# Performance work log

Hardware: AMD Instinct MI355X
Metric: run time of the kernel (lower is better)

## Reference

```python
import jax, jax.numpy as jnp
import numpy as np

N_EMBD = 1024
HEAD_SIZE = 64

def setup_inputs() -> dict:
    key = jax.random.key(0)
    kx, kk, kq, kv = jax.random.split(key, 4)
    x = jax.random.normal(kx, (8, 2048, N_EMBD), dtype=jnp.float32)
    scale = 1.0 / np.sqrt(N_EMBD)
    # nn.Linear weights are [out, in]; kaiming-uniform-ish init
    Wk = jax.random.uniform(kk, (HEAD_SIZE, N_EMBD), dtype=jnp.float32, minval=-scale, maxval=scale)
    Wq = jax.random.uniform(kq, (HEAD_SIZE, N_EMBD), dtype=jnp.float32, minval=-scale, maxval=scale)
    Wv = jax.random.uniform(kv, (HEAD_SIZE, N_EMBD), dtype=jnp.float32, minval=-scale, maxval=scale)
    return {"x": x, "Wk": Wk, "Wq": Wq, "Wv": Wv}

def reference(x, Wk, Wq, Wv):
    # x: [B, T, E]; W*: [H, E] (torch Linear layout)
    k = jnp.einsum('bte,he->bth', x, Wk)
    q = jnp.einsum('bte,he->bth', x, Wq)
    v = jnp.einsum('bte,he->bth', x, Wv)
    inv_sqrt_h = 1.0 / np.sqrt(HEAD_SIZE)
    wei = jnp.einsum('bth,bsh->bts', q, k) * inv_sqrt_h  # [B, T, T]
    wei = jax.nn.softmax(wei, axis=-1)
    out = jnp.einsum('bts,bsh->bth', wei, v)  # [B, T, H]
    return out
```

## Files before the change

kernel.cpp:

```cpp
#include <hip/hip_runtime.h>
#include <cstdint>

#define NB 8
#define TS 2048
#define NE 1024
#define HD 64
#define MTOT (NB*TS)

typedef float     f4  __attribute__((ext_vector_type(4)));
typedef short     s8v __attribute__((ext_vector_type(8)));
typedef short     s4v __attribute__((ext_vector_type(4)));
typedef int       i4v __attribute__((ext_vector_type(4)));
typedef _Float16  h8  __attribute__((ext_vector_type(8)));

__device__ __forceinline__ short f2bf(float f) {
  union { float f; uint32_t u; } x; x.f = f;
  return (short)((x.u + 0x7FFFu + ((x.u >> 16) & 1u)) >> 16);
}

__device__ __forceinline__ int pack2(float lo, float hi) {
  union { float f; uint32_t u; } a, b; a.f = lo; b.f = hi;
  return (int)__builtin_amdgcn_perm(b.u + 0x8000u, a.u + 0x8000u, 0x07060302u);
}

__device__ __forceinline__ void gl2lds(const void* gptr, void* lptr) {
  auto g = (const __attribute__((address_space(1))) uint32_t*)gptr;
  auto l = (__attribute__((address_space(3))) uint32_t*)lptr;
  __builtin_amdgcn_global_load_lds(g, l, 16, 0, 0);
}

template <int N>
__device__ __forceinline__ void wait_barrier() {
  asm volatile("s_waitcnt vmcnt(%0) lgkmcnt(0)" :: "n"(N) : "memory");
  __builtin_amdgcn_s_barrier();
}

__global__ __launch_bounds__(256) void wconv_kernel(
    const float* __restrict__ Wk, const float* __restrict__ Wq, const float* __restrict__ Wv,
    short* __restrict__ wb)
{
  const int idx = (blockIdx.x * 256 + threadIdx.x) * 4;
  const int p = idx >> 16;
  const int off = idx & 65535;
  const float* W = (p == 0) ? Wq : (p == 1) ? Wk : Wv;
  const float s = (p == 0) ? 0.18033688011112042f : 1.0f;
  const float4 v = *(const float4*)&W[off];
  s4v h; h[0] = f2bf(v.x*s); h[1] = f2bf(v.y*s); h[2] = f2bf(v.z*s); h[3] = f2bf(v.w*s);
  *(s4v*)&wb[idx] = h;
}

__global__ __launch_bounds__(256) void proj_kernel(
    const float* __restrict__ x, const short* __restrict__ wb,
    short* __restrict__ qo, short* __restrict__ ko, _Float16* __restrict__ vo)
{
  __shared__ float Xs[4][32][64];
  __shared__ short Ws[2][192][64];
  const int tid = threadIdx.x;
  const int wv = tid >> 6, lane = tid & 63, n = lane & 15, quad = lane >> 4;
  const int mg = wv & 1, cg = wv >> 1;
  const int r0 = blockIdx.x * 32;
  const int xrow = lane >> 4, xslot = lane & 15;
  const int wrow = lane >> 3, wslot = lane & 7;

  auto dmaX = [&](int c, int buf) {
#pragma unroll
    for (int u = 0; u < 2; ++u) {
      const int R0 = (wv * 2 + u) * 4;
      const int row = R0 + xrow;
      const int gs = (xslot + row) & 15;
      gl2lds(&x[(size_t)(r0 + row) * NE + c * 64 + gs * 4], &Xs[buf][R0][0]);
    }
  };
  auto dmaW = [&](int c, int buf) {
#pragma unroll
    for (int u = 0; u < 6; ++u) {
      const int C0 = (wv * 6 + u) * 8;
      const int col = C0 + wrow;
      const int gs = (wslot + col) & 7;
      gl2lds(&wb[(size_t)col * NE + c * 64 + gs * 8], &Ws[buf][C0][0]);
    }
  };

  const f4 fz = {0.f, 0.f, 0.f, 0.f};
  f4 acc[6] = {fz, fz, fz, fz, fz, fz};

  auto compute = [&](int bw, int bx) {
    s8v a[2];
    const int row = mg * 16 + n;
#pragma unroll
    for (int kc = 0; kc < 2; ++kc) {
      const int u0 = kc * 8 + quad * 2;
      const float* pr = &Xs[bx][row][0];
      const f4 f0 = *(const f4*)(pr + (((u0    ) - row) & 15) * 4);
      const f4 f1 = *(const f4*)(pr + (((u0 + 1) - row) & 15) * 4);
      i4v ai;
      ai[0] = pack2(f0[0], f0[1]); ai[1] = pack2(f0[2], f0[3]);
      ai[2] = pack2(f1[0], f1[1]); ai[3] = pack2(f1[2], f1[3]);
      a[kc] = __builtin_bit_cast(s8v, ai);
    }
#pragma unroll
    for (int nf = 0; nf < 6; ++nf) {
      const int col = cg * 96 + nf * 16 + n;
      const s8v b0 = *(const s8v*)&Ws[bw][col][(((0 + quad) - col) & 7) * 8];
      const s8v b1 = *(const s8v*)&Ws[bw][col][(((4 + quad) - col) & 7) * 8];
      acc[nf] = __builtin_amdgcn_mfma_f32_16x16x32_bf16(a[0], b0, acc[nf], 0, 0, 0);
      acc[nf] = __builtin_amdgcn_mfma_f32_16x16x32_bf16(a[1], b1, acc[nf], 0, 0, 0);
    }
  };

  dmaW(0, 0); dmaX(0, 0); dmaX(1, 1); dmaX(2, 2);
  wait_barrier<4>();

  for (int t = 0; t < 16; ++t) {
    if (t <= 14) dmaW(t + 1, (t + 1) & 1);
    if (t <= 12) dmaX(t + 3, (t + 3) & 3);
    compute(t & 1, t & 3);
    if (t <= 12)      wait_barrier<2>();
    else if (t <= 14) wait_barrier<0>();
  }

#pragma unroll
  for (int nf = 0; nf < 6; ++nf) {
    const int gc = cg * 96 + nf * 16;
    const int p = gc >> 6;
    const int rcol = (gc & 63) + n;
#pragma unroll
    for (int i = 0; i < 4; ++i) {
      const int R = r0 + mg * 16 + quad * 4 + i;
      const float av = acc[nf][i];
      if (p == 0)      qo[(size_t)R * HD + rcol] = f2bf(av);
      else if (p == 1) ko[(size_t)R * HD + rcol] = f2bf(av);
      else {
        const int t2 = R & (TS - 1), b = t2 & 31;
        const int pos = (t2 & ~31) | (((b >> 2) & 3) << 3) | (((b >> 4) & 1) << 2) | (b & 3);
        vo[(size_t)(R >> 11) * HD * TS + (size_t)rcol * TS + pos] = (_Float16)av;
      }
    }
  }
}

__global__ __launch_bounds__(512) void attn_kernel(
    const short* __restrict__ q, const short* __restrict__ k,
    const _Float16* __restrict__ vT, float* __restrict__ out)
{
  __shared__ __align__(16) char smem[98304];
  const int tid = threadIdx.x;
  const int wv = tid >> 6, lane = tid & 63, n = lane & 15, quad = lane >> 4;
  const int half = wv >> 2, qw = wv & 3;
  const int batch = blockIdx.x & 7;
  const int qg = blockIdx.x >> 3;
  const int m0 = batch * TS + qg * 64;
  const short*    kb = k  + (size_t)batch * TS * HD;
  const _Float16* vb = vT + (size_t)batch * HD * TS;
  const int drow = lane >> 3, dslot = lane & 7;
  const f4 fz = {0.f, 0.f, 0.f, 0.f};

  auto kbuf = [&](int buf) { return (short*)   (smem +         (half * 3 + buf) * 8192); };
  auto vbuf = [&](int buf) { return (_Float16*)(smem + 49152 + (half * 3 + buf) * 8192); };

  auto dmaKV = [&](int tt, int buf) {
    const int c = half * 16 + tt;
#pragma unroll
    for (int u = 0; u < 2; ++u) {
      const int K0 = (qw * 2 + u) * 8;
      const int key = K0 + drow;
      const int gs = (dslot + key) & 7;
      gl2lds(&kb[(size_t)(c * 64 + key) * HD + gs * 8], kbuf(buf) + K0 * 64);
    }
#pragma unroll
    for (int u = 0; u < 2; ++u) {
      const int D0 = (qw * 2 + u) * 8;
      const int d = D0 + drow;
      const int gs = (dslot + d) & 7;
      gl2lds(&vb[(size_t)d * TS + c * 64 + gs * 8], vbuf(buf) + D0 * 64);
    }
  };

  s8v qf[2];
#pragma unroll
  for (int kc = 0; kc < 2; ++kc)
    qf[kc] = *(const s8v*)&q[(size_t)(m0 + qw * 16 + n) * HD + kc * 32 + quad * 8];

  f4 o[4] = {fz, fz, fz, fz};
  f4 lD = fz;
  h8 ones;
#pragma unroll
  for (int j = 0; j < 8; ++j) ones[j] = (_Float16)1.0f;

  dmaKV(0, 0); dmaKV(1, 1);
  wait_barrier<4>();

  for (int t = 0; t < 16; ++t) {
    const int buf = t % 3;
    if (t <= 13) dmaKV(t + 2, (t + 2) % 3);

    const short*    ks = kbuf(buf);
    const _Float16* vs = vbuf(buf);

    s8v kf[4][2];
#pragma unroll
    for (int f = 0; f < 4; ++f)
#pragma unroll
      for (int kc = 0; kc < 2; ++kc) {
        const int key = f * 16 + n;
        kf[f][kc] = *(const s8v*)&ks[key * 64 + (((kc * 4 + quad) - key) & 7) * 8];
      }

    f4 st[4];
#pragma unroll
    for (int f = 0; f < 4; ++f) {
      st[f] = __builtin_amdgcn_mfma_f32_16x16x32_bf16(kf[f][0], qf[0], fz, 0, 0, 0);
      st[f] = __builtin_amdgcn_mfma_f32_16x16x32_bf16(kf[f][1], qf[1], st[f], 0, 0, 0);
    }

    h8 pa[2];
#pragma unroll
    for (int pr = 0; pr < 2; ++pr)
#pragma unroll
      for (int hf = 0; hf < 2; ++hf)
#pragma unroll
        for (int i = 0; i < 4; ++i)
          pa[pr][hf * 4 + i] = (_Float16)__builtin_amdgcn_exp2f(st[pr * 2 + hf][i]);

#pragma unroll
    for (int pr = 0; pr < 2; ++pr) {
      lD = __builtin_amdgcn_mfma_f32_16x16x32_f16(pa[pr], ones, lD, 0, 0, 0);
#pragma unroll
      for (int g = 0; g < 4; ++g) {
        const int d = g * 16 + n;
        const h8 vf = *(const h8*)&vs[d * 64 + (((pr * 4 + quad) - d) & 7) * 8];
        o[g] = __builtin_amdgcn_mfma_f32_16x16x32_f16(pa[pr], vf, o[g], 0, 0, 0);
      }
    }

    if (t <= 13)      wait_barrier<4>();
    else if (t == 14) wait_barrier<0>();
  }

  __syncthreads();

  float* o_c = (float*)smem;
  float* l_c = (float*)(smem + 36864);
  if (n == 0)
#pragma unroll
    for (int i = 0; i < 4; ++i) l_c[wv * 16 + quad * 4 + i] = lD[i];
#pragma unroll
  for (int g = 0; g < 4; ++g)
#pragma unroll
    for (int i = 0; i < 4; ++i)
      o_c[(wv * 16 + quad * 4 + i) * 68 + g * 16 + n] = o[g][i];
  __syncthreads();

#pragma unroll
  for (int rep = 0; rep < 2; ++rep) {
    const int idx = tid + rep * 512;
    const int qr = idx >> 4, d4 = (idx & 15) * 4;
    const int qw2 = qr >> 4, wr = qr & 15;
    const float L = l_c[qw2 * 16 + wr] + l_c[(qw2 + 4) * 16 + wr];
    const f4 s0 = *(const f4*)&o_c[(qw2 * 16 + wr) * 68 + d4];
    const f4 s1 = *(const f4*)&o_c[((qw2 + 4) * 16 + wr) * 68 + d4];
    f4 r = (s0 + s1);
    const float inv = 1.0f / L;
    r[0] *= inv; r[1] *= inv; r[2] *= inv; r[3] *= inv;
    *(f4*)&out[(size_t)(m0 + qr) * HD + d4] = r;
  }
}

extern "C" void kernel_launch(void* const* d_in, const int* in_sizes, int n_in,
                              void* d_out, int out_size, void* d_ws, size_t ws_size,
                              hipStream_t stream) {
  const float* x  = (const float*)d_in[0];
  const float* Wk = (const float*)d_in[1];
  const float* Wq = (const float*)d_in[2];
  const float* Wv = (const float*)d_in[3];
  float* out = (float*)d_out;

  short* qb = (short*)d_ws;
  short* kb = qb + (size_t)MTOT * HD;
  _Float16* vb = (_Float16*)(kb + (size_t)MTOT * HD);
  short* wb = (short*)(vb + (size_t)NB * HD * TS);

  wconv_kernel<<<192, 256, 0, stream>>>(Wk, Wq, Wv, wb);
  proj_kernel<<<MTOT / 32, 256, 0, stream>>>(x, wb, qb, kb, vb);
  attn_kernel<<<MTOT / 64, 512, 0, stream>>>(qb, kb, vb, out);
}
```

Baseline: 129.5 us.

## Split keys four ways across wave pairs, each wave handling 32 query rows

Reorganizes the attention block so the 8 waves form 4 key-range quarters of 2 waves each. Each wave now owns 32 query rows and processes 32-key tiles instead of 16 rows by 64 keys. Each K/V fragment loaded from LDS is reused across two query row tiles, which halves per-wave LDS reads per MFMA and shrinks per-buffer staging. The cost is that the final reduction combines four partial outputs per row instead of two, and more registers are held for accumulators.

```diff
diff --git a/kernel.cpp b/kernel.cpp
--- a/kernel.cpp
+++ b/kernel.cpp
@@ -146,93 +146,99 @@
   __shared__ __align__(16) char smem[98304];
   const int tid = threadIdx.x;
   const int wv = tid >> 6, lane = tid & 63, n = lane & 15, quad = lane >> 4;
-  const int half = wv >> 2, qw = wv & 3;
+  const int qtr = wv >> 1, qw = wv & 1;
   const int batch = blockIdx.x & 7;
   const int qg = blockIdx.x >> 3;
   const int m0 = batch * TS + qg * 64;
   const short*    kb = k  + (size_t)batch * TS * HD;
   const _Float16* vb = vT + (size_t)batch * HD * TS;
-  const int drow = lane >> 3, dslot = lane & 7;
   const f4 fz = {0.f, 0.f, 0.f, 0.f};
 
-  auto kbuf = [&](int buf) { return (short*)   (smem +         (half * 3 + buf) * 8192); };
-  auto vbuf = [&](int buf) { return (_Float16*)(smem + 49152 + (half * 3 + buf) * 8192); };
-
-  auto dmaKV = [&](int tt, int buf) {
-    const int c = half * 16 + tt;
+  auto kbuf = [&](int b) { return (short*)   (smem +         (qtr * 3 + b) * 4096); };
+  auto vbuf = [&](int b) { return (_Float16*)(smem + 49152 + (qtr * 3 + b) * 4096); };
+
+  auto dmaKV = [&](int t) {
+    const int b = t % 3;
+    const int c0 = qtr * 512 + t * 32;
 #pragma unroll
     for (int u = 0; u < 2; ++u) {
-      const int K0 = (qw * 2 + u) * 8;
-      const int key = K0 + drow;
-      const int gs = (dslot + key) & 7;
-      gl2lds(&kb[(size_t)(c * 64 + key) * HD + gs * 8], kbuf(buf) + K0 * 64);
+      const int K0 = qw * 16 + u * 8;
+      const int key = K0 + (lane >> 3);
+      const int s = lane & 7;
+      gl2lds(&kb[(size_t)(c0 + key) * HD + (((s + key) & 7) << 3)], kbuf(b) + K0 * 64);
     }
 #pragma unroll
     for (int u = 0; u < 2; ++u) {
-      const int D0 = (qw * 2 + u) * 8;
-      const int d = D0 + drow;
-      const int gs = (dslot + d) & 7;
-      gl2lds(&vb[(size_t)d * TS + c * 64 + gs * 8], vbuf(buf) + D0 * 64);
-    }
-  };
-
-  s8v qf[2];
-#pragma unroll
-  for (int kc = 0; kc < 2; ++kc)
-    qf[kc] = *(const s8v*)&q[(size_t)(m0 + qw * 16 + n) * HD + kc * 32 + quad * 8];
-
-  f4 o[4] = {fz, fz, fz, fz};
-  f4 lD = fz;
+      const int D0 = qw * 32 + u * 16;
+      const int d = D0 + (lane >> 2);
+      const int s = lane & 3;
+      gl2lds(&vb[(size_t)d * TS + c0 + (((s + d) & 3) << 3)], vbuf(b) + D0 * 32);
+    }
+  };
+
+  s8v qf[2][2];
+#pragma unroll
+  for (int m = 0; m < 2; ++m)
+#pragma unroll
+    for (int kc = 0; kc < 2; ++kc)
+      qf[m][kc] = *(const s8v*)&q[(size_t)(m0 + qw * 32 + m * 16 + n) * HD + kc * 32 + quad * 8];
+
+  f4 o[2][4];
+#pragma unroll
+  for (int m = 0; m < 2; ++m)
+#pragma unroll
+    for (int g = 0; g < 4; ++g) o[m][g] = fz;
+  f4 lD[2] = {fz, fz};
   h8 ones;
 #pragma unroll
   for (int j = 0; j < 8; ++j) ones[j] = (_Float16)1.0f;
 
-  dmaKV(0, 0); dmaKV(1, 1);
+  dmaKV(0); dmaKV(1);
   wait_barrier<4>();
 
   for (int t = 0; t < 16; ++t) {
-    const int buf = t % 3;
-    if (t <= 13) dmaKV(t + 2, (t + 2) % 3);
-
-    const short*    ks = kbuf(buf);
-    const _Float16* vs = vbuf(buf);
-
-    s8v kf[4][2];
-#pragma unroll
-    for (int f = 0; f < 4; ++f)
-#pragma unroll
-      for (int kc = 0; kc < 2; ++kc) {
-        const int key = f * 16 + n;
-        kf[f][kc] = *(const s8v*)&ks[key * 64 + (((kc * 4 + quad) - key) & 7) * 8];
-      }
-
-    f4 st[4];
-#pragma unroll
-    for (int f = 0; f < 4; ++f) {
-      st[f] = __builtin_amdgcn_mfma_f32_16x16x32_bf16(kf[f][0], qf[0], fz, 0, 0, 0);
-      st[f] = __builtin_amdgcn_mfma_f32_16x16x32_bf16(kf[f][1], qf[1], st[f], 0, 0, 0);
-    }
-
-    h8 pa[2];
-#pragma unroll
-    for (int pr = 0; pr < 2; ++pr)
-#pragma unroll
-      for (int hf = 0; hf < 2; ++hf)
-#pragma unroll
-        for (int i = 0; i < 4; ++i)
-          pa[pr][hf * 4 + i] = (_Float16)__builtin_amdgcn_exp2f(st[pr * 2 + hf][i]);
-
-#pragma unroll
-    for (int pr = 0; pr < 2; ++pr) {
-      lD = __builtin_amdgcn_mfma_f32_16x16x32_f16(pa[pr], ones, lD, 0, 0, 0);
+    if (t <= 13) dmaKV(t + 2);
+    {
+      const short*    ks = kbuf(t % 3);
+      const _Float16* vs = vbuf(t % 3);
+
+      s8v kf[2][2];
+#pragma unroll
+      for (int f = 0; f < 2; ++f)
+#pragma unroll
+        for (int kc = 0; kc < 2; ++kc) {
+          const int key = f * 16 + n;
+          kf[f][kc] = *(const s8v*)&ks[key * 64 + (((kc * 4 + quad) - key) & 7) * 8];
+        }
+
+      f4 st[2][2];
+#pragma unroll
+      for (int m = 0; m < 2; ++m)
+#pragma unroll
+        for (int f = 0; f < 2; ++f) {
+          st[m][f] = __builtin_amdgcn_mfma_f32_16x16x32_bf16(kf[f][0], qf[m][0], fz, 0, 0, 0);
+          st[m][f] = __builtin_amdgcn_mfma_f32_16x16x32_bf16(kf[f][1], qf[m][1], st[m][f], 0, 0, 0);
+        }
+
+      h8 pa[2];
+#pragma unroll
+      for (int m = 0; m < 2; ++m)
+#pragma unroll
+        for (int f = 0; f < 2; ++f)
+#pragma unroll
+          for (int i = 0; i < 4; ++i)
+            pa[m][f * 4 + i] = (_Float16)__builtin_amdgcn_exp2f(st[m][f][i]);
+
 #pragma unroll
       for (int g = 0; g < 4; ++g) {
         const int d = g * 16 + n;
-        const h8 vf = *(const h8*)&vs[d * 64 + (((pr * 4 + quad) - d) & 7) * 8];
-        o[g] = __builtin_amdgcn_mfma_f32_16x16x32_f16(pa[pr], vf, o[g], 0, 0, 0);
+        const h8 vf = *(const h8*)&vs[d * 32 + ((quad - d) & 3) * 8];
+        o[0][g] = __builtin_amdgcn_mfma_f32_16x16x32_f16(pa[0], vf, o[0][g], 0, 0, 0);
+        o[1][g] = __builtin_amdgcn_mfma_f32_16x16x32_f16(pa[1], vf, o[1][g], 0, 0, 0);
       }
-    }
-
+      lD[0] = __builtin_amdgcn_mfma_f32_16x16x32_f16(pa[0], ones, lD[0], 0, 0, 0);
+      lD[1] = __builtin_amdgcn_mfma_f32_16x16x32_f16(pa[1], ones, lD[1], 0, 0, 0);
+    }
     if (t <= 13)      wait_barrier<4>();
     else if (t == 14) wait_barrier<0>();
   }
@@ -240,30 +246,37 @@
   __syncthreads();
 
   float* o_c = (float*)smem;
-  float* l_c = (float*)(smem + 36864);
+  float* l_c = (float*)(smem + 69632);
   if (n == 0)
 #pragma unroll
-    for (int i = 0; i < 4; ++i) l_c[wv * 16 + quad * 4 + i] = lD[i];
-#pragma unroll
-  for (int g = 0; g < 4; ++g)
-#pragma unroll
-    for (int i = 0; i < 4; ++i)
-      o_c[(wv * 16 + quad * 4 + i) * 68 + g * 16 + n] = o[g][i];
+    for (int m = 0; m < 2; ++m)
+#pragma unroll
+      for (int i = 0; i < 4; ++i)
+        l_c[wv * 32 + m * 16 + quad * 4 + i] = lD[m][i];
+#pragma unroll
+  for (int m = 0; m < 2; ++m)
+#pragma unroll
+    for (int g = 0; g < 4; ++g)
+#pragma unroll
+      for (int i = 0; i < 4; ++i)
+        o_c[(wv * 32 + m * 16 + quad * 4 + i) * 68 + g * 16 + n] = o[m][g][i];
   __syncthreads();
 
-#pragma unroll
-  for (int rep = 0; rep < 2; ++rep) {
-    const int idx = tid + rep * 512;
-    const int qr = idx >> 4, d4 = (idx & 15) * 4;
-    const int qw2 = qr >> 4, wr = qr & 15;
-    const float L = l_c[qw2 * 16 + wr] + l_c[(qw2 + 4) * 16 + wr];
-    const f4 s0 = *(const f4*)&o_c[(qw2 * 16 + wr) * 68 + d4];
-    const f4 s1 = *(const f4*)&o_c[((qw2 + 4) * 16 + wr) * 68 + d4];
-    f4 r = (s0 + s1);
-    const float inv = 1.0f / L;
-    r[0] *= inv; r[1] *= inv; r[2] *= inv; r[3] *= inv;
-    *(f4*)&out[(size_t)(m0 + qr) * HD + d4] = r;
-  }
+  const int qr = tid >> 3, d8 = (tid & 7) * 8;
+  const int qw2 = qr >> 5, r32 = qr & 31;
+  float L = 0.f;
+  f4 s0 = fz, s1 = fz;
+#pragma unroll
+  for (int qt = 0; qt < 4; ++qt) {
+    const int w = qt * 2 + qw2;
+    L  += l_c[w * 32 + r32];
+    s0 += *(const f4*)&o_c[(w * 32 + r32) * 68 + d8];
+    s1 += *(const f4*)&o_c[(w * 32 + r32) * 68 + d8 + 4];
+  }
+  const float inv = 1.0f / L;
+  s0 *= inv; s1 *= inv;
+  *(f4*)&out[(size_t)(m0 + qr) * HD + d8]     = s0;
+  *(f4*)&out[(size_t)(m0 + qr) * HD + d8 + 4] = s1;
 }
 
 extern "C" void kernel_launch(void* const* d_in, const int* in_sizes, int n_in,
```

Result: no change. 130.7 us (+0.9%).
